# Kernel optimization log

Hardware: AMD Instinct MI355X
Metric: run time of the kernel (lower is better)

The kernel has to match this reference:

```python
import jax, jax.numpy as jnp
import numpy as np

N, D, K, G = 262144, 256, 1024, 4
C = D // G
BETA = 0.5


def setup_inputs() -> dict:
    key = jax.random.key(0)
    k1, k2 = jax.random.split(key)
    z = jax.random.normal(k1, (N, D), dtype=jnp.float32)
    # original init: uniform(-1/K, 1/K)
    codebooks = jax.random.uniform(k2, (G, K, C), dtype=jnp.float32,
                                   minval=-1.0 / K, maxval=1.0 / K)
    return {"z": z, "codebooks": codebooks}


def reference(z, codebooks):
    # z: [N, D] -> [N, G, C]; codebooks: [G, K, C]
    zg = z.reshape(-1, G, C)
    # squared distances: ||z||^2 + ||e||^2 - 2 z.e  -> [N, G, K]
    z_sq = jnp.sum(zg ** 2, axis=-1, keepdims=True)            # [N, G, 1]
    e_sq = jnp.sum(codebooks ** 2, axis=-1)                    # [G, K]
    dots = jnp.einsum('ngc,gkc->ngk', zg, codebooks)           # [N, G, K]
    d = z_sq + e_sq[None, :, :] - 2.0 * dots
    idx = jnp.argmin(d, axis=-1)                               # [N, G]
    # gather codes: [N, G, C]
    zq = codebooks[jnp.arange(G)[None, :], idx]
    # per-group VQ loss, averaged over groups (means over N and C per group)
    sg = jax.lax.stop_gradient
    commit = jnp.mean((sg(zq) - zg) ** 2, axis=(0, 2))         # [G]
    embed = jnp.mean((zq - sg(zg)) ** 2, axis=(0, 2))          # [G]
    loss = jnp.mean(BETA * commit + embed)
    # straight-through estimator
    zq_st = zg + sg(zq - zg)
    return zq_st.reshape(-1, D), loss
```

## Files before the change

kernel.cpp:

```cpp
#include <hip/hip_runtime.h>
#include <hip/hip_fp16.h>
#include <stdint.h>

typedef _Float16 f16;
typedef f16   f16x8 __attribute__((ext_vector_type(8)));
typedef float f32x4 __attribute__((ext_vector_type(4)));

#define NTOK 262144
#define DDIM 256
#define KCB  1024
#define GG   4
#define CC   64
#define FR   8
#define ROWS_PER_BLK (FR * 16 * 4)
#define NBLKX (NTOK / ROWS_PER_BLK)
#define NPART (NBLKX * GG)
#define TILE_K 64
#define NTILE  (KCB / TILE_K)
#define TILE_B (TILE_K * CC * 2)

static __device__ __forceinline__ uint32_t umin32(uint32_t a, uint32_t b) { return a < b ? a : b; }

typedef __attribute__((address_space(1))) const void gv_t;
typedef __attribute__((address_space(3))) void lv_t;
static __device__ __forceinline__ void gl_lds16(const void* g, void* l) {
    __builtin_amdgcn_global_load_lds((gv_t*)g, (lv_t*)l, 16, 0, 0);
}
static __device__ __forceinline__ void gl_lds4(const void* g, void* l) {
    __builtin_amdgcn_global_load_lds((gv_t*)g, (lv_t*)l, 4, 0, 0);
}

__global__ __launch_bounds__(64) void vq_prep(const float* __restrict__ cb,
                                              f16* __restrict__ cb16,
                                              float* __restrict__ esq05) {
    int gk = blockIdx.x;
    int c  = threadIdx.x;
    float v = cb[(size_t)gk * CC + c];
    cb16[(size_t)gk * CC + c] = (f16)v;
    float s = v * v;
    #pragma unroll
    for (int off = 32; off; off >>= 1) s += __shfl_down(s, off, 64);
    if (c == 0) esq05[gk] = 0.5f + s;
}

__global__ __launch_bounds__(256, 3) void vq_main(const float* __restrict__ z,
                                                  const float* __restrict__ cb32,
                                                  const f16* __restrict__ cb16,
                                                  const float* __restrict__ esq05,
                                                  float* __restrict__ out,
                                                  float* __restrict__ part) {
    const int lane = threadIdx.x & 63;
    const int w    = threadIdx.x >> 6;
    const int g    = blockIdx.y;
    const int r0   = blockIdx.x * ROWS_PER_BLK + w * (FR * 16);
    const int q    = lane >> 4;
    const int t    = lane & 15;

    __shared__ __align__(16) char sb[2][TILE_B + 256];
    __shared__ float ls[4];

    const f16*   cbg = cb16  + (size_t)g * KCB * CC;
    const float* eg  = esq05 + (size_t)g * KCB;

    auto stage = [&](int tile, int bufsel) {
        const char* gtile = (const char*)cbg + (size_t)tile * TILE_B;
        #pragma unroll
        for (int c2 = 0; c2 < 2; ++c2) {
            uint32_t x  = (uint32_t)(w * 2048 + c2 * 1024 + lane * 16);
            uint32_t gx = x ^ (((x >> 7) & 7u) << 4);
            gl_lds16(gtile + gx, &sb[bufsel][w * 2048 + c2 * 1024]);
        }
        if (w == 0) gl_lds4(eg + tile * TILE_K + lane, &sb[bufsel][TILE_B]);
    };

    stage(0, 0);

    f16x8 a[FR][2];
    float zsq[FR];
    #pragma unroll
    for (int f = 0; f < FR; ++f) {
        int row = r0 + f * 16 + t;
        const float* zp = z + (size_t)row * DDIM + g * CC + q * 8;
        float4 v0 = *(const float4*)(zp);
        float4 v1 = *(const float4*)(zp + 4);
        float4 v2 = *(const float4*)(zp + 32);
        float4 v3 = *(const float4*)(zp + 36);
        f16x8 a0 = { (f16)(-2.f*v0.x),(f16)(-2.f*v0.y),(f16)(-2.f*v0.z),(f16)(-2.f*v0.w),
                     (f16)(-2.f*v1.x),(f16)(-2.f*v1.y),(f16)(-2.f*v1.z),(f16)(-2.f*v1.w) };
        f16x8 a1 = { (f16)(-2.f*v2.x),(f16)(-2.f*v2.y),(f16)(-2.f*v2.z),(f16)(-2.f*v2.w),
                     (f16)(-2.f*v3.x),(f16)(-2.f*v3.y),(f16)(-2.f*v3.z),(f16)(-2.f*v3.w) };
        a[f][0] = a0; a[f][1] = a1;
        float s = v0.x*v0.x + v0.y*v0.y + v0.z*v0.z + v0.w*v0.w
                + v1.x*v1.x + v1.y*v1.y + v1.z*v1.z + v1.w*v1.w
                + v2.x*v2.x + v2.y*v2.y + v2.z*v2.z + v2.w*v2.w
                + v3.x*v3.x + v3.y*v3.y + v3.z*v3.z + v3.w*v3.w;
        s += __shfl_xor(s, 16, 64);
        s += __shfl_xor(s, 32, 64);
        zsq[f] = s;
    }

    uint32_t run[FR][4];
    #pragma unroll
    for (int f = 0; f < FR; ++f)
        #pragma unroll
        for (int i = 0; i < 4; ++i) run[f][i] = 0xFFFFFFFFu;

    const uint32_t binner = (uint32_t)t * 128 + (((uint32_t)(q * 16)) ^ (((uint32_t)(t & 7)) << 4));

    for (int tt = 0; tt < NTILE; ++tt) {
        __syncthreads();
        if (tt + 1 < NTILE) stage(tt + 1, (tt + 1) & 1);
        const char*  bb = sb[tt & 1];
        const float* eb = (const float*)(sb[tt & 1] + TILE_B);
        #pragma unroll
        for (int sub = 0; sub < 4; ++sub) {
            f16x8 b0 = *(const f16x8*)(bb + sub * 2048 + binner);
            f16x8 b1 = *(const f16x8*)(bb + sub * 2048 + (binner ^ 64));
            float e  = eb[sub * 16 + t];
            f32x4 ce = { e, e, e, e };
            uint32_t code = (uint32_t)(tt * TILE_K + sub * 16 + t);
            #pragma unroll
            for (int f = 0; f < FR; ++f) {
                f32x4 acc = __builtin_amdgcn_mfma_f32_16x16x32_f16(a[f][0], b0, ce, 0, 0, 0);
                acc = __builtin_amdgcn_mfma_f32_16x16x32_f16(a[f][1], b1, acc, 0, 0, 0);
                #pragma unroll
                for (int i = 0; i < 4; ++i) {
                    uint32_t k = (__float_as_uint(acc[i]) & 0xFFFFFC00u) | code;
                    run[f][i] = umin32(run[f][i], k);
                }
            }
        }
    }

    float lsum = 0.0f;
    #pragma unroll
    for (int f = 0; f < FR; ++f) {
        #pragma unroll
        for (int i = 0; i < 4; ++i) {
            uint32_t k = run[f][i];
            k = umin32(k, __shfl_xor(k, 1, 64));
            k = umin32(k, __shfl_xor(k, 2, 64));
            k = umin32(k, __shfl_xor(k, 4, 64));
            k = umin32(k, __shfl_xor(k, 8, 64));
            int   kw     = (int)(k & 1023u);
            float minval = __uint_as_float(k & 0xFFFFFC00u) - 0.5f;
            int rloc = q * 4 + i;
            int grow = r0 + f * 16 + rloc;
            const float4* src = (const float4*)(cb32 + ((size_t)(g * KCB + kw)) * CC) + t;
            float4*       dst = (float4*)(out + (size_t)grow * DDIM + g * CC) + t;
            *dst = *src;
            float zs = __shfl(zsq[f], rloc, 64);
            if (t == 0) lsum += zs + minval;
        }
    }
    #pragma unroll
    for (int off = 32; off; off >>= 1) lsum += __shfl_down(lsum, off, 64);

    if (lane == 0) ls[w] = lsum;
    __syncthreads();
    if (threadIdx.x == 0) {
        part[blockIdx.y * NBLKX + blockIdx.x] = ls[0] + ls[1] + ls[2] + ls[3];
    }
}

__global__ __launch_bounds__(256) void vq_final(const float* __restrict__ part,
                                                float* __restrict__ out_loss) {
    __shared__ float ls[4];
    float s = 0.0f;
    for (int i = threadIdx.x; i < NPART; i += 256) s += part[i];
    #pragma unroll
    for (int off = 32; off; off >>= 1) s += __shfl_down(s, off, 64);
    int lane = threadIdx.x & 63, w = threadIdx.x >> 6;
    if (lane == 0) ls[w] = s;
    __syncthreads();
    if (threadIdx.x == 0) {
        *out_loss = 1.5f * (ls[0] + ls[1] + ls[2] + ls[3]) * (1.0f / ((float)NTOK * (float)DDIM));
    }
}

extern "C" void kernel_launch(void* const* d_in, const int* in_sizes, int n_in,
                              void* d_out, int out_size, void* d_ws, size_t ws_size,
                              hipStream_t stream) {
    const float* z  = (const float*)d_in[0];
    const float* cb = (const float*)d_in[1];
    float* out = (float*)d_out;

    char* ws = (char*)d_ws;
    f16*   cb16  = (f16*)ws;
    float* esq05 = (float*)(ws + (size_t)GG * KCB * CC * sizeof(f16));
    float* part  = (float*)(ws + (size_t)GG * KCB * CC * sizeof(f16)
                               + (size_t)GG * KCB * sizeof(float));

    vq_prep<<<GG * KCB, 64, 0, stream>>>(cb, cb16, esq05);

    dim3 grid(NBLKX, GG);
    vq_main<<<grid, 256, 0, stream>>>(z, cb, cb16, esq05, out, part);

    vq_final<<<1, 256, 0, stream>>>(part, out + (size_t)NTOK * DDIM);
}
```

Before: 224.4 us.

## Split VQ into argmin and gather kernels, halve rows per wave, batch MFMAs

The fused kernel becomes two. An argmin kernel computes nearest-code indices and the loss partials, then writes 16-bit indices to the workspace. A separate grid-stride gather kernel copies the fp32 codebook rows to the output. Rows per wave drop from 8 to 4 fragments, and launch bounds rise to 4 blocks per CU. MFMAs are grouped under raised wave priority. The intent is to cut register pressure and raise occupancy for the compute phase, and to make the output writes fully coalesced. The cost is an extra launch, an index round trip through memory, and codebook tiles being reloaded for twice as many blocks.

Result: slower. 233.2 us (+3.9%).

```diff
diff --git a/kernel.cpp b/kernel.cpp
--- a/kernel.cpp
+++ b/kernel.cpp
@@ -11,7 +11,7 @@
 #define KCB  1024
 #define GG   4
 #define CC   64
-#define FR   8
+#define FR   4
 #define ROWS_PER_BLK (FR * 16 * 4)
 #define NBLKX (NTOK / ROWS_PER_BLK)
 #define NPART (NBLKX * GG)
@@ -43,12 +43,11 @@
     if (c == 0) esq05[gk] = 0.5f + s;
 }
 
-__global__ __launch_bounds__(256, 3) void vq_main(const float* __restrict__ z,
-                                                  const float* __restrict__ cb32,
-                                                  const f16* __restrict__ cb16,
-                                                  const float* __restrict__ esq05,
-                                                  float* __restrict__ out,
-                                                  float* __restrict__ part) {
+__global__ __launch_bounds__(256, 4) void vq_argmin(const float* __restrict__ z,
+                                                    const f16* __restrict__ cb16,
+                                                    const float* __restrict__ esq05,
+                                                    unsigned short* __restrict__ idx,
+                                                    float* __restrict__ part) {
     const int lane = threadIdx.x & 63;
     const int w    = threadIdx.x >> 6;
     const int g    = blockIdx.y;
@@ -62,18 +61,19 @@
     const f16*   cbg = cb16  + (size_t)g * KCB * CC;
     const float* eg  = esq05 + (size_t)g * KCB;
 
-    auto stage = [&](int tile, int bufsel) {
-        const char* gtile = (const char*)cbg + (size_t)tile * TILE_B;
-        #pragma unroll
-        for (int c2 = 0; c2 < 2; ++c2) {
-            uint32_t x  = (uint32_t)(w * 2048 + c2 * 1024 + lane * 16);
-            uint32_t gx = x ^ (((x >> 7) & 7u) << 4);
-            gl_lds16(gtile + gx, &sb[bufsel][w * 2048 + c2 * 1024]);
-        }
-        if (w == 0) gl_lds4(eg + tile * TILE_K + lane, &sb[bufsel][TILE_B]);
-    };
-
-    stage(0, 0);
+    #define STAGE(tile, bufsel)                                                      \
+        do {                                                                         \
+            const char* gtile = (const char*)cbg + (size_t)(tile) * TILE_B;          \
+            _Pragma("unroll")                                                        \
+            for (int c2 = 0; c2 < 2; ++c2) {                                         \
+                uint32_t x  = (uint32_t)(w * 2048 + c2 * 1024 + lane * 16);          \
+                uint32_t gx = x ^ (((x >> 7) & 7u) << 4);                            \
+                gl_lds16(gtile + gx, &sb[bufsel][w * 2048 + c2 * 1024]);             \
+            }                                                                        \
+            if (w == 0) gl_lds4(eg + (tile) * TILE_K + lane, &sb[bufsel][TILE_B]);   \
+        } while (0)
+
+    STAGE(0, 0);
 
     f16x8 a[FR][2];
     float zsq[FR];
@@ -109,7 +109,7 @@
 
     for (int tt = 0; tt < NTILE; ++tt) {
         __syncthreads();
-        if (tt + 1 < NTILE) stage(tt + 1, (tt + 1) & 1);
+        if (tt + 1 < NTILE) STAGE(tt + 1, (tt + 1) & 1);
         const char*  bb = sb[tt & 1];
         const float* eb = (const float*)(sb[tt & 1] + TILE_B);
         #pragma unroll
@@ -119,13 +119,20 @@
             float e  = eb[sub * 16 + t];
             f32x4 ce = { e, e, e, e };
             uint32_t code = (uint32_t)(tt * TILE_K + sub * 16 + t);
+            f32x4 acc[FR];
+            __builtin_amdgcn_s_setprio(1);
+            #pragma unroll
+            for (int f = 0; f < FR; ++f)
+                acc[f] = __builtin_amdgcn_mfma_f32_16x16x32_f16(a[f][0], b0, ce, 0, 0, 0);
+            #pragma unroll
+            for (int f = 0; f < FR; ++f)
+                acc[f] = __builtin_amdgcn_mfma_f32_16x16x32_f16(a[f][1], b1, acc[f], 0, 0, 0);
+            __builtin_amdgcn_s_setprio(0);
             #pragma unroll
             for (int f = 0; f < FR; ++f) {
-                f32x4 acc = __builtin_amdgcn_mfma_f32_16x16x32_f16(a[f][0], b0, ce, 0, 0, 0);
-                acc = __builtin_amdgcn_mfma_f32_16x16x32_f16(a[f][1], b1, acc, 0, 0, 0);
                 #pragma unroll
                 for (int i = 0; i < 4; ++i) {
-                    uint32_t k = (__float_as_uint(acc[i]) & 0xFFFFFC00u) | code;
+                    uint32_t k = (__float_as_uint(acc[f][i]) & 0xFFFFFC00u) | code;
                     run[f][i] = umin32(run[f][i], k);
                 }
             }
@@ -146,11 +153,11 @@
             float minval = __uint_as_float(k & 0xFFFFFC00u) - 0.5f;
             int rloc = q * 4 + i;
             int grow = r0 + f * 16 + rloc;
-            const float4* src = (const float4*)(cb32 + ((size_t)(g * KCB + kw)) * CC) + t;
-            float4*       dst = (float4*)(out + (size_t)grow * DDIM + g * CC) + t;
-            *dst = *src;
             float zs = __shfl(zsq[f], rloc, 64);
-            if (t == 0) lsum += zs + minval;
+            if (t == 0) {
+                idx[(grow << 2) | g] = (unsigned short)kw;
+                lsum += zs + minval;
+            }
         }
     }
     #pragma unroll
@@ -160,6 +167,22 @@
     __syncthreads();
     if (threadIdx.x == 0) {
         part[blockIdx.y * NBLKX + blockIdx.x] = ls[0] + ls[1] + ls[2] + ls[3];
+    }
+}
+
+__global__ __launch_bounds__(256) void vq_gather(const unsigned short* __restrict__ idx,
+                                                 const float* __restrict__ cb32,
+                                                 float* __restrict__ out) {
+    const int stride = gridDim.x * 256;
+    const int total  = NTOK * (DDIM / 4);
+    for (int i = blockIdx.x * 256 + threadIdx.x; i < total; i += stride) {
+        int row = i >> 6;
+        int d4  = i & 63;
+        int g   = d4 >> 4;
+        int c4  = d4 & 15;
+        int k   = idx[(row << 2) | g];
+        float4 v = *(const float4*)(cb32 + (size_t)(((g << 10) + k) << 6) + (c4 << 2));
+        *(float4*)(out + ((size_t)row << 8) + (d4 << 2)) = v;
     }
 }
 
@@ -188,13 +211,15 @@
     char* ws = (char*)d_ws;
     f16*   cb16  = (f16*)ws;
     float* esq05 = (float*)(ws + (size_t)GG * KCB * CC * sizeof(f16));
-    float* part  = (float*)(ws + (size_t)GG * KCB * CC * sizeof(f16)
-                               + (size_t)GG * KCB * sizeof(float));
+    float* part  = (float*)(ws + 512*1024 + 16*1024);
+    unsigned short* idx = (unsigned short*)(ws + 512*1024 + 32*1024);
 
     vq_prep<<<GG * KCB, 64, 0, stream>>>(cb, cb16, esq05);
 
     dim3 grid(NBLKX, GG);
-    vq_main<<<grid, 256, 0, stream>>>(z, cb, cb16, esq05, out, part);
+    vq_argmin<<<grid, 256, 0, stream>>>(z, cb16, esq05, idx, part);
+
+    vq_gather<<<4096, 256, 0, stream>>>(idx, cb, out);
 
     vq_final<<<1, 256, 0, stream>>>(part, out + (size_t)NTOK * DDIM);
 }
```
